# Optimization experiments

Measured on AMD Instinct MI355X. Metric: run time of the kernel, lower is better.

## Reference

```python
import jax, jax.numpy as jnp
import numpy as np

N = 50000        # nodes
E = 1600000      # edges
NFEAT = 128      # node feature dim
NEDGE = 16       # raw edge feature dim
NHID = 128
NLAYER = 4
NGRAPH = 512
NOUT = 128
BN_EPS = 1e-5


def _bn(h, g, b):
    # eval-mode BatchNorm1d with running_mean=0, running_var=1
    return h * (g / jnp.sqrt(1.0 + BN_EPS)) + b


def setup_inputs() -> dict:
    key = jax.random.key(0)
    ks = jax.random.split(key, 24)
    s = 0.05
    inp = {
        "x": jax.random.normal(ks[0], (N, NFEAT), jnp.float32),
        "edge_index": jax.random.randint(ks[1], (2, E), 0, N, jnp.int64),
        "edge_attr": jax.random.normal(ks[2], (E, NEDGE), jnp.float32),
        "batch": jnp.sort(jax.random.randint(ks[3], (N,), 0, NGRAPH, jnp.int64)),
        # input encoder MLP (Linear + BN + ReLU)
        "in_W": jax.random.normal(ks[4], (NFEAT, NHID), jnp.float32) * s,
        "in_b": jnp.zeros((NHID,), jnp.float32),
        "in_g": jnp.ones((NHID,), jnp.float32),
        "in_beta": jnp.zeros((NHID,), jnp.float32),
        # per-layer edge encoder MLPs
        "edge_W": jax.random.normal(ks[5], (NLAYER, NEDGE, NHID), jnp.float32) * s,
        "edge_b": jnp.zeros((NLAYER, NHID), jnp.float32),
        "edge_g": jnp.ones((NLAYER, NHID), jnp.float32),
        "edge_beta": jnp.zeros((NLAYER, NHID), jnp.float32),
        # per-layer GINEConv linear (bias=False since bn=True) and eps
        "conv_W": jax.random.normal(ks[6], (NLAYER, NHID, NHID), jnp.float32) * s,
        "eps": jnp.zeros((NLAYER,), jnp.float32),
        # per-layer BatchNorm after conv
        "bn_g": jnp.ones((NLAYER, NHID), jnp.float32),
        "bn_b": jnp.zeros((NLAYER, NHID), jnp.float32),
        # output encoder: 2-layer MLP, norm after layer 1, no final activation
        "out_W1": jax.random.normal(ks[7], (NHID, NHID), jnp.float32) * s,
        "out_b1": jnp.zeros((NHID,), jnp.float32),
        "out_g1": jnp.ones((NHID,), jnp.float32),
        "out_beta1": jnp.zeros((NHID,), jnp.float32),
        "out_W2": jax.random.normal(ks[8], (NHID, NOUT), jnp.float32) * s,
        "out_b2": jnp.zeros((NOUT,), jnp.float32),
    }
    return inp


def reference(x, edge_index, edge_attr, batch,
              in_W, in_b, in_g, in_beta,
              edge_W, edge_b, edge_g, edge_beta,
              conv_W, eps, bn_g, bn_b,
              out_W1, out_b1, out_g1, out_beta1,
              out_W2, out_b2):
    # input encoder (MLP, 1 layer: Linear + BN + ReLU)
    h = jax.nn.relu(_bn(x @ in_W + in_b, in_g, in_beta))
    prev = h
    src, dst = edge_index[0], edge_index[1]
    for l in range(NLAYER):
        # edge encoder
        ea = jax.nn.relu(_bn(edge_attr @ edge_W[l] + edge_b[l], edge_g[l], edge_beta[l]))
        # GINEConv: messages relu(x_src + e), sum-aggregate to dst
        m = jax.nn.relu(h[src] + ea)                         # [E, NHID]
        agg = jax.ops.segment_sum(m, dst, num_segments=N)    # [N, NHID]
        h = ((1.0 + eps[l]) * h + agg) @ conv_W[l]
        h = jax.nn.relu(_bn(h, bn_g[l], bn_b[l]))            # dropout=0
        h = h + prev                                         # residual
        prev = h
    # add pooling over graphs
    pooled = jax.ops.segment_sum(h, batch, num_segments=NGRAPH)  # [NGRAPH, NHID]
    # output encoder: Linear+BN+ReLU, then Linear
    o = jax.nn.relu(_bn(pooled @ out_W1 + out_b1, out_g1, out_beta1))
    return o @ out_W2 + out_b2
```

## Files before the change

### kernel.cpp

```cpp
#include <hip/hip_runtime.h>
#include <stdint.h>

typedef uint32_t u32;
typedef _Float16 h2v __attribute__((ext_vector_type(2)));
typedef __attribute__((ext_vector_type(8))) short bf16x8;
typedef __attribute__((ext_vector_type(4))) float f32x4;

#define NGRAPH 512

__device__ __forceinline__ float uif(u32 u) { return __builtin_bit_cast(float, u); }
__device__ __forceinline__ u32 fiu(float f) { return __builtin_bit_cast(u32, f); }
__device__ __forceinline__ unsigned short bf16r(float f) {
    return (unsigned short)((fiu(f) + 0x8000u) >> 16);
}
__device__ __forceinline__ u32 pack_bf16(float lo, float hi) {
    return ((fiu(lo) + 0x8000u) >> 16) | ((fiu(hi) + 0x8000u) & 0xFFFF0000u);
}
__device__ __forceinline__ u32 pkh(float a, float b) {
    unsigned short la = __builtin_bit_cast(unsigned short, (_Float16)a);
    unsigned short hb = __builtin_bit_cast(unsigned short, (_Float16)b);
    return (u32)la | ((u32)hb << 16);
}
__device__ __forceinline__ float fdot2w(u32 a, u32 b, float c) {
#if __has_builtin(__builtin_amdgcn_fdot2)
    return __builtin_amdgcn_fdot2(__builtin_bit_cast(h2v, a),
                                  __builtin_bit_cast(h2v, b), c, false);
#else
    h2v av = __builtin_bit_cast(h2v, a), bv = __builtin_bit_cast(h2v, b);
    return c + (float)av[0]*(float)bv[0] + (float)av[1]*(float)bv[1];
#endif
}

__global__ __launch_bounds__(256) void prep_kernel(
    const float* __restrict__ in_b, const float* __restrict__ in_g, const float* __restrict__ in_beta,
    const float* __restrict__ edge_W,
    const float* __restrict__ edge_b, const float* __restrict__ edge_g, const float* __restrict__ edge_beta,
    const float* __restrict__ bn_g, const float* __restrict__ bn_b,
    const float* __restrict__ out_b1, const float* __restrict__ out_g1, const float* __restrict__ out_beta1,
    float* __restrict__ consts, u32* __restrict__ wpk)
{
    int c = threadIdx.x;
    if (c >= 128) return;
    const float rs = rsqrtf(1.0f + 1e-5f);
    float es = in_g[c] * rs;
    consts[c]       = es;
    consts[128 + c] = in_b[c] * es + in_beta[c];
    for (int l = 0; l < 4; ++l) {
        float s = edge_g[l*128 + c] * rs;
        consts[256  + l*128 + c] = s;
        consts[768  + l*128 + c] = edge_b[l*128 + c] * s + edge_beta[l*128 + c];
        float bs = bn_g[l*128 + c] * rs;
        consts[1280 + l*128 + c] = bs;
        consts[1792 + l*128 + c] = bn_b[l*128 + c];
        for (int kk = 0; kk < 8; ++kk) {
            float w0 = edge_W[(l*16 + 2*kk)*128 + c];
            float w1 = edge_W[(l*16 + 2*kk + 1)*128 + c];
            wpk[(l*8 + kk)*128 + c] = pkh(w0, w1);
        }
    }
    float s1 = out_g1[c] * rs;
    consts[2304 + c] = s1;
    consts[2432 + c] = out_b1[c] * s1 + out_beta1[c];
}

__global__ __launch_bounds__(256) void prepw_kernel(
    const float* __restrict__ in_W, const float* __restrict__ conv_W,
    unsigned short* __restrict__ WtAll)
{
    for (int idx = blockIdx.x*blockDim.x + threadIdx.x; idx < 5*128*128;
         idx += gridDim.x*blockDim.x) {
        int w = idx >> 14, rem = idx & 16383;
        int nn = rem >> 7, kk = rem & 127;
        const float* S = (w == 0) ? in_W : conv_W + (size_t)(w-1)*16384;
        WtAll[idx] = bf16r(S[kk*128 + nn]);
    }
}

__global__ __launch_bounds__(256) void xconv_kernel(
    const float* __restrict__ x, u32* __restrict__ x16, int n4)
{
    for (int i = blockIdx.x*blockDim.x + threadIdx.x; i < n4;
         i += gridDim.x*blockDim.x) {
        float4 v = *(const float4*)(x + (size_t)i*4);
        uint2 o; o.x = pack_bf16(v.x, v.y); o.y = pack_bf16(v.z, v.w);
        *(uint2*)(x16 + (size_t)i*2) = o;
    }
}

__global__ __launch_bounds__(256) void count_kernel(
    const int* __restrict__ dst, int E, int* __restrict__ cnt)
{
    for (int e = blockIdx.x*blockDim.x + threadIdx.x; e < E; e += gridDim.x*blockDim.x)
        atomicAdd(&cnt[dst[e]], 1);
}

__global__ __launch_bounds__(1024) void scan_kernel(
    const int* __restrict__ cnt, int n, int E,
    int* __restrict__ offs, int* __restrict__ cursor)
{
    __shared__ int sh[1024];
    const int t = threadIdx.x;
    const int chunk = (n + 1023) >> 10;
    const int lo = t * chunk;
    const int hi = min(n, lo + chunk);
    int s = 0;
    for (int i = lo; i < hi; ++i) s += cnt[i];
    sh[t] = s;
    __syncthreads();
    for (int d = 1; d < 1024; d <<= 1) {
        int v = (t >= d) ? sh[t - d] : 0;
        __syncthreads();
        sh[t] += v;
        __syncthreads();
    }
    int base = sh[t] - s;
    for (int i = lo; i < hi; ++i) { int c = cnt[i]; offs[i] = base; cursor[i] = base; base += c; }
    if (t == 1023) offs[n] = E;
}

__global__ __launch_bounds__(256) void scatter_kernel(
    const int* __restrict__ src, const int* __restrict__ dst,
    const float* __restrict__ attr, int E,
    int* __restrict__ cursor, int* __restrict__ srcoff, uint4* __restrict__ attrp)
{
    const int T = gridDim.x * blockDim.x;
    const int tid = blockIdx.x*blockDim.x + threadIdx.x;
    int e[4]; int p[4];
    #pragma unroll
    for (int k = 0; k < 4; ++k) e[k] = tid + k*T;
    #pragma unroll
    for (int k = 0; k < 4; ++k)
        if (e[k] < E) p[k] = atomicAdd(&cursor[dst[e[k]]], 1);
    #pragma unroll
    for (int k = 0; k < 4; ++k) {
        if (e[k] >= E) continue;
        const int ee = e[k], pp = p[k];
        srcoff[pp] = src[ee] * 256;
        const float4* ar = (const float4*)(attr + (size_t)ee*16);
        float4 v0 = ar[0], v1 = ar[1], v2 = ar[2], v3 = ar[3];
        uint4 o0, o1;
        o0.x = pkh(v0.x, v0.y); o0.y = pkh(v0.z, v0.w);
        o0.z = pkh(v1.x, v1.y); o0.w = pkh(v1.z, v1.w);
        o1.x = pkh(v2.x, v2.y); o1.y = pkh(v2.z, v2.w);
        o1.z = pkh(v3.x, v3.y); o1.w = pkh(v3.z, v3.w);
        attrp[2*(size_t)pp] = o0; attrp[2*(size_t)pp + 1] = o1;
    }
}

__global__ __launch_bounds__(256) void goff_kernel(
    const int* __restrict__ batch, int n, int* __restrict__ goff)
{
    int g = blockIdx.x*blockDim.x + threadIdx.x;
    if (g > NGRAPH) return;
    if (g == NGRAPH) { goff[NGRAPH] = n; return; }
    int lo = 0, hi = n;
    while (lo < hi) { int m = (lo + hi) >> 1; if (batch[m] < g) lo = m + 1; else hi = m; }
    goff[g] = lo;
}

__global__ __launch_bounds__(256) void agg_kernel(
    const char* __restrict__ hb,
    const uint4* __restrict__ attrp,
    const int* __restrict__ srcoff,
    const int* __restrict__ offs,
    const u32* __restrict__ wpk,
    const float* __restrict__ escale, const float* __restrict__ eoff,
    const float* __restrict__ epsp, int layer,
    u32* __restrict__ C16, int n)
{
    const int wave = threadIdx.x >> 6, lane = threadIdx.x & 63;
    const int lane4 = lane * 4;
    const int c0 = lane * 2;
    u32 wA[8], wB[8];
    #pragma unroll
    for (int kk = 0; kk < 8; ++kk) {
        wA[kk] = wpk[(layer*8 + kk)*128 + c0];
        wB[kk] = wpk[(layer*8 + kk)*128 + c0 + 1];
    }
    const float sc0 = escale[c0], sc1 = escale[c0+1];
    const float of0 = eoff[c0],   of1 = eoff[c0+1];
    const float epsv = 1.0f + epsp[layer];

    for (int node = blockIdx.x*4 + wave; node < n; node += gridDim.x*4) {
        const int beg = offs[node], end = offs[node+1];
        float acc0 = 0.f, acc1 = 0.f;

        auto edge = [&](int idx) {
            const int iu = __builtin_amdgcn_readfirstlane(idx);
            const uint4 q0 = attrp[2*(size_t)iu];
            const uint4 q1 = attrp[2*(size_t)iu + 1];
            const int so = srcoff[iu];
            const u32 hv = *(const u32*)(hb + so + lane4);
            float r0 = 0.f, r1 = 0.f;
            r0 = fdot2w(q0.x, wA[0], r0); r1 = fdot2w(q0.x, wB[0], r1);
            r0 = fdot2w(q0.y, wA[1], r0); r1 = fdot2w(q0.y, wB[1], r1);
            r0 = fdot2w(q0.z, wA[2], r0); r1 = fdot2w(q0.z, wB[2], r1);
            r0 = fdot2w(q0.w, wA[3], r0); r1 = fdot2w(q0.w, wB[3], r1);
            r0 = fdot2w(q1.x, wA[4], r0); r1 = fdot2w(q1.x, wB[4], r1);
            r0 = fdot2w(q1.y, wA[5], r0); r1 = fdot2w(q1.y, wB[5], r1);
            r0 = fdot2w(q1.z, wA[6], r0); r1 = fdot2w(q1.z, wB[6], r1);
            r0 = fdot2w(q1.w, wA[7], r0); r1 = fdot2w(q1.w, wB[7], r1);
            float ea0 = fmaxf(fmaf(r0, sc0, of0), 0.f);
            float ea1 = fmaxf(fmaf(r1, sc1, of1), 0.f);
            float h0 = uif(hv << 16);
            float h1 = uif(hv & 0xFFFF0000u);
            acc0 += fmaxf(h0 + ea0, 0.f);
            acc1 += fmaxf(h1 + ea1, 0.f);
        };

        int i = beg;
        for (; i + 1 < end; i += 2) { edge(i); edge(i + 1); }
        if (i < end) edge(i);

        const u32 hn = *(const u32*)(hb + (size_t)node*256 + lane4);
        float t0 = fmaf(epsv, uif(hn << 16), acc0);
        float t1 = fmaf(epsv, uif(hn & 0xFFFF0000u), acc1);
        C16[(size_t)node*64 + lane] = pack_bf16(t0, t1);
    }
}

__global__ __launch_bounds__(256) void conv_mfma_kernel(
    const unsigned short* X16, int M,
    const unsigned short* __restrict__ Wt,
    const float* __restrict__ scale, const float* __restrict__ off,
    const unsigned short* __restrict__ resid16,
    unsigned short* out16, int do_relu)
{
    __shared__ unsigned short Ws[128*128];
    for (int i = threadIdx.x*8; i < 128*128; i += 256*8) {
        int row = i >> 7;
        int bo = (i & 127) * 2;
        int4 v = *(const int4*)(Wt + i);
        *(int4*)((char*)Ws + row*256 + (bo ^ ((row & 7) << 4))) = v;
    }
    __syncthreads();
    const int wave = threadIdx.x >> 6, lane = threadIdx.x & 63;
    const int row0 = blockIdx.x*64 + wave*16;
    const int l15 = lane & 15, l4 = lane >> 4;
    int arow = row0 + l15; if (arow > M-1) arow = M-1;
    const unsigned short* ap = X16 + (size_t)arow*128 + l4*8;
    f32x4 acc[8];
    #pragma unroll
    for (int t = 0; t < 8; ++t) acc[t] = f32x4{0.f, 0.f, 0.f, 0.f};
    #pragma unroll
    for (int ks = 0; ks < 4; ++ks) {
        bf16x8 a = *(const bf16x8*)(ap + ks*32);
        #pragma unroll
        for (int t = 0; t < 8; ++t) {
            int brow = t*16 + l15;
            int bo = ks*64 + l4*16;
            bf16x8 b = *(const bf16x8*)((const char*)Ws + brow*256 + (bo ^ ((brow & 7) << 4)));
            acc[t] = __builtin_amdgcn_mfma_f32_16x16x32_bf16(a, b, acc[t], 0, 0, 0);
        }
    }
    #pragma unroll
    for (int t = 0; t < 8; ++t) {
        int col = t*16 + l15;
        float sc = scale[col], of = off[col];
        #pragma unroll
        for (int r = 0; r < 4; ++r) {
            int row = row0 + l4*4 + r;
            if (row < M) {
                float y = fmaf(acc[t][r], sc, of);
                if (do_relu) y = fmaxf(y, 0.f);
                if (resid16) y += uif((u32)resid16[(size_t)row*128 + col] << 16);
                out16[(size_t)row*128 + col] = bf16r(y);
            }
        }
    }
}

__global__ __launch_bounds__(256) void pool_kernel(
    const u32* __restrict__ h16, const int* __restrict__ goff,
    float* __restrict__ pooled)
{
    const int wave = threadIdx.x >> 6, lane = threadIdx.x & 63;
    const int g = blockIdx.x*4 + wave;
    if (g >= NGRAPH) return;
    float ax = 0.f, ay = 0.f;
    const int beg = goff[g], end = goff[g+1];
    for (int node = beg; node < end; ++node) {
        u32 v = h16[(size_t)node*64 + lane];
        ax += uif(v << 16); ay += uif(v & 0xFFFF0000u);
    }
    *(float2*)&pooled[g*128 + lane*2] = make_float2(ax, ay);
}

__global__ __launch_bounds__(256) void gemm128_kernel(
    const float* __restrict__ in, int rows,
    const float* __restrict__ W,
    const float* __restrict__ scale, const float* __restrict__ off,
    float* out, int do_relu)
{
    __shared__ float Wsh[128*128];
    for (int i = threadIdx.x*4; i < 128*128; i += 256*4)
        *(float4*)&Wsh[i] = *(const float4*)&W[i];
    __syncthreads();
    const int wave = threadIdx.x >> 6, lane = threadIdx.x & 63;
    const int c0 = lane * 2;
    const float sc0 = scale ? scale[c0]   : 1.0f;
    const float sc1 = scale ? scale[c0+1] : 1.0f;
    const float of0 = off ? off[c0]   : 0.0f;
    const float of1 = off ? off[c0+1] : 0.0f;
    for (int rp = blockIdx.x*4 + wave; rp*2 < rows; rp += gridDim.x*4) {
        const int row0 = __builtin_amdgcn_readfirstlane(rp * 2);
        const float* xr = in + (size_t)row0 * 128;
        float a00 = 0.f, a01 = 0.f, a10 = 0.f, a11 = 0.f;
        #pragma unroll 8
        for (int k = 0; k < 128; ++k) {
            float x0 = xr[k];
            float x1 = xr[128 + k];
            float2 w = *(const float2*)&Wsh[k*128 + c0];
            a00 = fmaf(x0, w.x, a00); a01 = fmaf(x0, w.y, a01);
            a10 = fmaf(x1, w.x, a10); a11 = fmaf(x1, w.y, a11);
        }
        float y00 = fmaf(a00, sc0, of0), y01 = fmaf(a01, sc1, of1);
        float y10 = fmaf(a10, sc0, of0), y11 = fmaf(a11, sc1, of1);
        if (do_relu) {
            y00 = fmaxf(y00, 0.f); y01 = fmaxf(y01, 0.f);
            y10 = fmaxf(y10, 0.f); y11 = fmaxf(y11, 0.f);
        }
        *(float2*)&out[(size_t)row0*128 + c0]     = make_float2(y00, y01);
        *(float2*)&out[(size_t)(row0+1)*128 + c0] = make_float2(y10, y11);
    }
}

extern "C" void kernel_launch(void* const* d_in, const int* in_sizes, int n_in,
                              void* d_out, int out_size, void* d_ws, size_t ws_size,
                              hipStream_t stream)
{
    const float* x         = (const float*)d_in[0];
    const int*   eidx      = (const int*)d_in[1];
    const float* eattr     = (const float*)d_in[2];
    const int*   batch     = (const int*)d_in[3];
    const float* in_W      = (const float*)d_in[4];
    const float* in_b      = (const float*)d_in[5];
    const float* in_g      = (const float*)d_in[6];
    const float* in_beta   = (const float*)d_in[7];
    const float* edge_W    = (const float*)d_in[8];
    const float* edge_b    = (const float*)d_in[9];
    const float* edge_g    = (const float*)d_in[10];
    const float* edge_beta = (const float*)d_in[11];
    const float* conv_W    = (const float*)d_in[12];
    const float* epsp      = (const float*)d_in[13];
    const float* bn_g      = (const float*)d_in[14];
    const float* bn_b      = (const float*)d_in[15];
    const float* out_W1    = (const float*)d_in[16];
    const float* out_b1    = (const float*)d_in[17];
    const float* out_g1    = (const float*)d_in[18];
    const float* out_beta1 = (const float*)d_in[19];
    const float* out_W2    = (const float*)d_in[20];
    const float* out_b2    = (const float*)d_in[21];

    const int N = in_sizes[0] / 128;
    const int E = in_sizes[1] / 2;
    const int* src = eidx;
    const int* dst = eidx + E;

    char* ws = (char*)d_ws;
    size_t o = 0;
    auto alloc = [&](size_t bytes) { void* p = ws + o; o = (o + bytes + 255) & ~(size_t)255; return p; };
    unsigned short* P    = (unsigned short*)alloc((size_t)N * 128 * 2);
    unsigned short* Q    = (unsigned short*)alloc((size_t)N * 128 * 2);
    uint4* attrp         = (uint4*)alloc((size_t)E * 32);
    int*   srcoff        = (int*)alloc((size_t)E * 4);
    int*   offs          = (int*)alloc((size_t)(N + 1) * 4);
    int*   cursor        = (int*)alloc((size_t)N * 4);
    int*   cnt           = (int*)alloc((size_t)N * 4);
    int*   goff          = (int*)alloc((NGRAPH + 1) * 4);
    float* pooled        = (float*)alloc(NGRAPH * 128 * 4);
    float* o1            = (float*)alloc(NGRAPH * 128 * 4);
    float* consts        = (float*)alloc(2560 * 4);
    u32*   wpk           = (u32*)alloc(4 * 8 * 128 * 4);
    unsigned short* WtAll = (unsigned short*)alloc(5 * 128 * 128 * 2);

    prep_kernel<<<1, 256, 0, stream>>>(in_b, in_g, in_beta, edge_W,
                                       edge_b, edge_g, edge_beta,
                                       bn_g, bn_b, out_b1, out_g1, out_beta1,
                                       consts, wpk);
    prepw_kernel<<<80, 256, 0, stream>>>(in_W, conv_W, WtAll);
    xconv_kernel<<<2048, 256, 0, stream>>>(x, (u32*)Q, N * 32);

    (void)hipMemsetAsync(cnt, 0, (size_t)N * 4, stream);
    count_kernel<<<2048, 256, 0, stream>>>(dst, E, cnt);
    scan_kernel<<<1, 1024, 0, stream>>>(cnt, N, E, offs, cursor);
    scatter_kernel<<<2048, 256, 0, stream>>>(src, dst, eattr, E, cursor, srcoff, attrp);
    goff_kernel<<<3, 256, 0, stream>>>(batch, N, goff);

    const int gblocks = (N + 63) / 64;
    conv_mfma_kernel<<<gblocks, 256, 0, stream>>>(Q, N, WtAll,
                                                  consts, consts + 128,
                                                  nullptr, Q, 1);

    unsigned short* cur = Q;
    unsigned short* oth = P;
    for (int l = 0; l < 4; ++l) {
        agg_kernel<<<2048, 256, 0, stream>>>((const char*)cur, attrp, srcoff, offs,
                                             wpk,
                                             consts + 256 + l*128,
                                             consts + 768 + l*128,
                                             epsp, l, (u32*)oth, N);
        conv_mfma_kernel<<<gblocks, 256, 0, stream>>>(oth, N,
                                                      WtAll + (size_t)(1 + l)*16384,
                                                      consts + 1280 + l*128,
                                                      consts + 1792 + l*128,
                                                      cur, oth, 1);
        unsigned short* t = cur; cur = oth; oth = t;
    }

    pool_kernel<<<128, 256, 0, stream>>>((const u32*)cur, goff, pooled);

    gemm128_kernel<<<64, 256, 0, stream>>>(pooled, NGRAPH, out_W1,
                                           consts + 2304, consts + 2432, o1, 1);
    gemm128_kernel<<<64, 256, 0, stream>>>(o1, NGRAPH, out_W2,
                                           nullptr, out_b2, (float*)d_out, 0);
}
```

Before: 926.0 us.

## Split edge-message sum and compute edge encoder with MFMA per node

Result: slower. 970.7 us (+4.8%).

```diff
diff --git a/kernel.cpp b/kernel.cpp
--- a/kernel.cpp
+++ b/kernel.cpp
@@ -4,6 +4,7 @@
 typedef uint32_t u32;
 typedef _Float16 h2v __attribute__((ext_vector_type(2)));
 typedef __attribute__((ext_vector_type(8))) short bf16x8;
+typedef __attribute__((ext_vector_type(8))) _Float16 f16x8_t;
 typedef __attribute__((ext_vector_type(4))) float f32x4;
 
 #define NGRAPH 512
@@ -21,23 +22,13 @@
     unsigned short hb = __builtin_bit_cast(unsigned short, (_Float16)b);
     return (u32)la | ((u32)hb << 16);
 }
-__device__ __forceinline__ float fdot2w(u32 a, u32 b, float c) {
-#if __has_builtin(__builtin_amdgcn_fdot2)
-    return __builtin_amdgcn_fdot2(__builtin_bit_cast(h2v, a),
-                                  __builtin_bit_cast(h2v, b), c, false);
-#else
-    h2v av = __builtin_bit_cast(h2v, a), bv = __builtin_bit_cast(h2v, b);
-    return c + (float)av[0]*(float)bv[0] + (float)av[1]*(float)bv[1];
-#endif
-}
 
 __global__ __launch_bounds__(256) void prep_kernel(
     const float* __restrict__ in_b, const float* __restrict__ in_g, const float* __restrict__ in_beta,
-    const float* __restrict__ edge_W,
     const float* __restrict__ edge_b, const float* __restrict__ edge_g, const float* __restrict__ edge_beta,
     const float* __restrict__ bn_g, const float* __restrict__ bn_b,
     const float* __restrict__ out_b1, const float* __restrict__ out_g1, const float* __restrict__ out_beta1,
-    float* __restrict__ consts, u32* __restrict__ wpk)
+    float* __restrict__ consts)
 {
     int c = threadIdx.x;
     if (c >= 128) return;
@@ -52,15 +43,21 @@
         float bs = bn_g[l*128 + c] * rs;
         consts[1280 + l*128 + c] = bs;
         consts[1792 + l*128 + c] = bn_b[l*128 + c];
-        for (int kk = 0; kk < 8; ++kk) {
-            float w0 = edge_W[(l*16 + 2*kk)*128 + c];
-            float w1 = edge_W[(l*16 + 2*kk + 1)*128 + c];
-            wpk[(l*8 + kk)*128 + c] = pkh(w0, w1);
-        }
     }
     float s1 = out_g1[c] * rs;
     consts[2304 + c] = s1;
     consts[2432 + c] = out_b1[c] * s1 + out_beta1[c];
+}
+
+__global__ __launch_bounds__(256) void wfrag_kernel(
+    const float* __restrict__ edge_W, _Float16* __restrict__ wfrag)
+{
+    int idx = blockIdx.x*blockDim.x + threadIdx.x;
+    if (idx >= 4*8*64*8) return;
+    int j = idx & 7, lane = (idx >> 3) & 63, t = (idx >> 9) & 7, l = idx >> 12;
+    int k = (lane >> 4)*8 + j;
+    int n = t*16 + (lane & 15);
+    wfrag[idx] = (k < 16) ? (_Float16)edge_W[(l*16 + k)*128 + n] : (_Float16)0.f;
 }
 
 __global__ __launch_bounds__(256) void prepw_kernel(
@@ -163,54 +160,89 @@
     const uint4* __restrict__ attrp,
     const int* __restrict__ srcoff,
     const int* __restrict__ offs,
-    const u32* __restrict__ wpk,
+    const _Float16* __restrict__ wfrag,
     const float* __restrict__ escale, const float* __restrict__ eoff,
     const float* __restrict__ epsp, int layer,
     u32* __restrict__ C16, int n)
 {
+    __shared__ float eabuf[4][128];
     const int wave = threadIdx.x >> 6, lane = threadIdx.x & 63;
     const int lane4 = lane * 4;
     const int c0 = lane * 2;
-    u32 wA[8], wB[8];
-    #pragma unroll
-    for (int kk = 0; kk < 8; ++kk) {
-        wA[kk] = wpk[(layer*8 + kk)*128 + c0];
-        wB[kk] = wpk[(layer*8 + kk)*128 + c0 + 1];
-    }
-    const float sc0 = escale[c0], sc1 = escale[c0+1];
-    const float of0 = eoff[c0],   of1 = eoff[c0+1];
+    const int l15 = lane & 15, l4 = lane >> 4;
+
+    f16x8_t bw[8];
+    #pragma unroll
+    for (int t = 0; t < 8; ++t)
+        bw[t] = *(const f16x8_t*)(wfrag + ((size_t)(layer*8 + t)*64 + lane)*8);
+    float sc[8], of[8];
+    #pragma unroll
+    for (int t = 0; t < 8; ++t) {
+        sc[t] = escale[l15 + 16*t];
+        of[t] = eoff[l15 + 16*t];
+    }
     const float epsv = 1.0f + epsp[layer];
+    const f16x8_t az = (f16x8_t)(_Float16)0.f;
 
     for (int node = blockIdx.x*4 + wave; node < n; node += gridDim.x*4) {
         const int beg = offs[node], end = offs[node+1];
-        float acc0 = 0.f, acc1 = 0.f;
-
-        auto edge = [&](int idx) {
+
+        float easum[8];
+        #pragma unroll
+        for (int t = 0; t < 8; ++t) easum[t] = 0.f;
+        for (int g = beg; g < end; g += 16) {
+            const int rem = end - g;
+            f16x8_t a = az;
+            if (l4 < 2) {
+                int e = g + l15; if (e > end - 1) e = end - 1;
+                a = *(const f16x8_t*)((const char*)attrp + (size_t)e*32 + l4*16);
+            }
+            if (rem >= 16) {
+                #pragma unroll
+                for (int t = 0; t < 8; ++t) {
+                    f32x4 d = __builtin_amdgcn_mfma_f32_16x16x32_f16(
+                        a, bw[t], f32x4{0.f,0.f,0.f,0.f}, 0, 0, 0);
+                    #pragma unroll
+                    for (int r = 0; r < 4; ++r)
+                        easum[t] += fmaxf(fmaf(d[r], sc[t], of[t]), 0.f);
+                }
+            } else {
+                #pragma unroll
+                for (int t = 0; t < 8; ++t) {
+                    f32x4 d = __builtin_amdgcn_mfma_f32_16x16x32_f16(
+                        a, bw[t], f32x4{0.f,0.f,0.f,0.f}, 0, 0, 0);
+                    #pragma unroll
+                    for (int r = 0; r < 4; ++r) {
+                        float y = fmaxf(fmaf(d[r], sc[t], of[t]), 0.f);
+                        easum[t] += ((l4*4 + r) < rem) ? y : 0.f;
+                    }
+                }
+            }
+        }
+        #pragma unroll
+        for (int t = 0; t < 8; ++t) {
+            float v = easum[t];
+            v += __shfl_xor(v, 16);
+            v += __shfl_xor(v, 32);
+            easum[t] = v;
+        }
+        if (l4 == 0) {
+            #pragma unroll
+            for (int t = 0; t < 8; ++t)
+                eabuf[wave][t*16 + l15] = easum[t];
+        }
+        float2 ea2 = *(float2*)&eabuf[wave][c0];
+
+        float acc0 = ea2.x, acc1 = ea2.y;
+        auto hedge = [&](int idx) {
             const int iu = __builtin_amdgcn_readfirstlane(idx);
-            const uint4 q0 = attrp[2*(size_t)iu];
-            const uint4 q1 = attrp[2*(size_t)iu + 1];
-            const int so = srcoff[iu];
-            const u32 hv = *(const u32*)(hb + so + lane4);
-            float r0 = 0.f, r1 = 0.f;
-            r0 = fdot2w(q0.x, wA[0], r0); r1 = fdot2w(q0.x, wB[0], r1);
-            r0 = fdot2w(q0.y, wA[1], r0); r1 = fdot2w(q0.y, wB[1], r1);
-            r0 = fdot2w(q0.z, wA[2], r0); r1 = fdot2w(q0.z, wB[2], r1);
-            r0 = fdot2w(q0.w, wA[3], r0); r1 = fdot2w(q0.w, wB[3], r1);
-            r0 = fdot2w(q1.x, wA[4], r0); r1 = fdot2w(q1.x, wB[4], r1);
-            r0 = fdot2w(q1.y, wA[5], r0); r1 = fdot2w(q1.y, wB[5], r1);
-            r0 = fdot2w(q1.z, wA[6], r0); r1 = fdot2w(q1.z, wB[6], r1);
-            r0 = fdot2w(q1.w, wA[7], r0); r1 = fdot2w(q1.w, wB[7], r1);
-            float ea0 = fmaxf(fmaf(r0, sc0, of0), 0.f);
-            float ea1 = fmaxf(fmaf(r1, sc1, of1), 0.f);
-            float h0 = uif(hv << 16);
-            float h1 = uif(hv & 0xFFFF0000u);
-            acc0 += fmaxf(h0 + ea0, 0.f);
-            acc1 += fmaxf(h1 + ea1, 0.f);
+            const u32 hv = *(const u32*)(hb + srcoff[iu] + lane4);
+            acc0 += uif(hv << 16);
+            acc1 += uif(hv & 0xFFFF0000u);
         };
-
         int i = beg;
-        for (; i + 1 < end; i += 2) { edge(i); edge(i + 1); }
-        if (i < end) edge(i);
+        for (; i + 1 < end; i += 2) { hedge(i); hedge(i + 1); }
+        if (i < end) hedge(i);
 
         const u32 hn = *(const u32*)(hb + (size_t)node*256 + lane4);
         float t0 = fmaf(epsv, uif(hn << 16), acc0);
@@ -371,13 +403,14 @@
     float* pooled        = (float*)alloc(NGRAPH * 128 * 4);
     float* o1            = (float*)alloc(NGRAPH * 128 * 4);
     float* consts        = (float*)alloc(2560 * 4);
-    u32*   wpk           = (u32*)alloc(4 * 8 * 128 * 4);
+    _Float16* wfrag      = (_Float16*)alloc(4 * 8 * 64 * 8 * 2);
     unsigned short* WtAll = (unsigned short*)alloc(5 * 128 * 128 * 2);
 
-    prep_kernel<<<1, 256, 0, stream>>>(in_b, in_g, in_beta, edge_W,
+    prep_kernel<<<1, 256, 0, stream>>>(in_b, in_g, in_beta,
                                        edge_b, edge_g, edge_beta,
                                        bn_g, bn_b, out_b1, out_g1, out_beta1,
-                                       consts, wpk);
+                                       consts);
+    wfrag_kernel<<<64, 256, 0, stream>>>(edge_W, wfrag);
     prepw_kernel<<<80, 256, 0, stream>>>(in_W, conv_W, WtAll);
     xconv_kernel<<<2048, 256, 0, stream>>>(x, (u32*)Q, N * 32);
 
@@ -396,7 +429,7 @@
     unsigned short* oth = P;
     for (int l = 0; l < 4; ++l) {
         agg_kernel<<<2048, 256, 0, stream>>>((const char*)cur, attrp, srcoff, offs,
-                                             wpk,
+                                             wfrag,
                                              consts + 256 + l*128,
                                              consts + 768 + l*128,
                                              epsp, l, (u32*)oth, N);
```
